# Kernel optimization log

Hardware: AMD Instinct MI355X
Metric: run time of the kernel (lower is better)

Reference implementation:

```python
import jax, jax.numpy as jnp
from jax import lax
import numpy as np

V, E, L, B = 50257, 512, 2048, 8
BASE_RATIO, MIN_RATIO = 0.5, 0.1

def next_power_of_two(x):
    return 1 if x == 0 else 2 ** ((x - 1).bit_length())

def setup_inputs() -> dict:
    key = jax.random.key(0)
    ks = jax.random.split(key, 9)
    s = 0.02
    return {
        "x": jax.random.randint(ks[0], (B, L), 0, V),
        "Wtok": jax.random.normal(ks[1], (V, E), jnp.float32) * s,
        "Wpos": jax.random.normal(ks[2], (L, E), jnp.float32) * s,
        "Wc1": jax.random.normal(ks[3], (3, E, E), jnp.float32) * s,  # WIO layout
        "bc1": jnp.zeros((E,), jnp.float32),
        "Wc2": jax.random.normal(ks[4], (3, E, E), jnp.float32) * s,
        "bc2": jnp.zeros((E,), jnp.float32),
        "Wp": jax.random.normal(ks[5], (E, E), jnp.float32) * (1.0 / np.sqrt(E)),  # torch Linear weight [out,in]
        "bp": jnp.zeros((E,), jnp.float32),
    }

def _conv1d(h, W, b):
    # h: [B, L, E] (NWC), W: [k, in, out] (WIO), SAME padding == torch padding=1 for k=3
    y = lax.conv_general_dilated(h, W, (1,), "SAME", dimension_numbers=("NWC", "WIO", "NWC"))
    return jax.nn.relu(y + b)

def reference(x, Wtok, Wpos, Wc1, bc1, Wc2, bc2, Wp, bp):
    Bsz, Ls = x.shape
    # token + position embedding
    h = Wtok[x] + Wpos[jnp.arange(Ls)][None, :, :]          # [B, L, E]
    h = _conv1d(h, Wc1, bc1)
    h = _conv1d(h, Wc2, bc2)
    # pad to next power of two along sequence
    P = next_power_of_two(Ls)
    if P > Ls:
        h = jnp.pad(h, ((0, 0), (0, P - Ls), (0, 0)))
    x_fft = jnp.fft.fft(h, axis=1)                          # [B, P, E] complex64
    mag = jnp.abs(x_fft)
    thr = 0.1 * mag.max(axis=1, keepdims=True)
    complexity = (mag > thr).astype(jnp.float32).mean(axis=(1, 2))   # [B]
    ratio = jnp.clip(BASE_RATIO * (1.0 - complexity), MIN_RATIO, 1.0)
    N = jnp.clip((ratio * Ls).astype(jnp.int32), 1, Ls)     # [B] kept freq count
    # vectorized equivalent of the per-sample truncation loop:
    # keep first N[i] frequencies (zero the rest), then ifft with n=Ls
    fmask = jnp.arange(Ls)[None, :] < N[:, None]            # [B, L] bool
    x_fft_c = jnp.where(fmask[:, :, None], x_fft[:, :Ls, :], 0.0)
    x_ifft = jnp.fft.ifft(x_fft_c, n=Ls, axis=1).real.astype(h.dtype)  # [B, L, E]
    out = x_ifft @ Wp.T + bp                                # proj
    # recon_target is the exact same computation in the original module
    recon_target = out
    mask_f = fmask.astype(out.dtype)[:, :, None]            # [B, L, 1]
    diff = jnp.abs(out - recon_target) * mask_f
    denom = mask_f.sum() * E
    loss_recon = diff.sum() / jnp.maximum(denom, 1.0)
    return out, loss_recon
```

## Files before the change

kernel.cpp:

```cpp
#include <hip/hip_runtime.h>
#include <hip/hip_bf16.h>
#include <cstddef>

#define BB 8
#define LL 2048
#define EE 512
#define KCONV 1536
#define LPAD 2050

typedef _Float16 h16;
typedef _Float16 h16x2 __attribute__((ext_vector_type(2)));
typedef _Float16 h16x4 __attribute__((ext_vector_type(4)));
typedef _Float16 h16x8 __attribute__((ext_vector_type(8)));
typedef float    f32x4 __attribute__((ext_vector_type(4)));

static const size_t OFF_WT1  = 0;
static const size_t OFF_WT2  = 1572864;
static const size_t OFF_WPB  = 3145728;
static const size_t OFF_CNT2 = 3670016;
static const size_t OFF_H0P  = 4194304;
static const size_t OFF_H1P  = 20987904;
static const size_t OFF_H2T  = 37781504;
static const size_t OFF_XF   = 4194304;
static const size_t OFF_H3E  = 54558720;
static const size_t OFF_H3T  = 20987904;
static const size_t WS_NEED  = 71335936;

__device__ __forceinline__ int padi(int i) { return i + (i >> 5); }
__device__ __forceinline__ int dr5(int n) {
    return ((n & 3) << 8) | (((n >> 2) & 3) << 6) | (((n >> 4) & 3) << 4)
         | (((n >> 6) & 3) << 2) | ((n >> 8) & 3);
}
#define TWOPI_2048 0.0030679616f

__global__ __launch_bounds__(256) void prep_embed_kernel(
    const float* __restrict__ Wc1, const float* __restrict__ Wc2,
    const float* __restrict__ Wp,
    h16* __restrict__ Wt1, h16* __restrict__ Wt2, h16* __restrict__ Wpb,
    const int* __restrict__ x, const float* __restrict__ Wtok,
    const float* __restrict__ Wpos, h16* __restrict__ h0p, h16* __restrict__ h1p)
{
    int blk = blockIdx.x, t = threadIdx.x;
    __shared__ float tl[64][65];
    if (blk < 384) {
        const float* src = (blk < 192) ? Wc1 : Wc2;
        h16* dst = (blk < 192) ? Wt1 : Wt2;
        int tile = blk % 192;
        int o0 = (tile / 24) * 64, r0 = (tile % 24) * 64;
        #pragma unroll
        for (int it = 0; it < 4; ++it) {
            int idx = it * 256 + t;
            int rr = idx >> 4, oo4 = (idx & 15) * 4;
            f32x4 v = *(const f32x4*)(src + (size_t)(r0 + rr) * 512 + o0 + oo4);
            tl[rr][oo4] = v[0]; tl[rr][oo4 + 1] = v[1];
            tl[rr][oo4 + 2] = v[2]; tl[rr][oo4 + 3] = v[3];
        }
        __syncthreads();
        #pragma unroll
        for (int it = 0; it < 4; ++it) {
            int idx = it * 256 + t;
            int oo = idx & 63, rr4 = (idx >> 6) * 4;
            h16x4 v;
            v.x = (h16)tl[rr4][oo]; v.y = (h16)tl[rr4 + 1][oo];
            v.z = (h16)tl[rr4 + 2][oo]; v.w = (h16)tl[rr4 + 3][oo];
            *(h16x4*)(dst + (size_t)(o0 + oo) * 1536 + r0 + rr4) = v;
        }
    } else if (blk < 448) {
        int base = (blk - 384) * 4096;
        #pragma unroll
        for (int i = 0; i < 4; ++i) {
            int idx = base + (i * 256 + t) * 4;
            f32x4 a = *(const f32x4*)(Wp + idx);
            h16x4 v; v.x = (h16)a[0]; v.y = (h16)a[1]; v.z = (h16)a[2]; v.w = (h16)a[3];
            *(h16x4*)(Wpb + idx) = v;
        }
    } else {
        int rowg = (blk - 448) * 4 + (t >> 6);
        int b = rowg / LPAD, r = rowg % LPAD;
        int lane = t & 63;
        size_t o = (size_t)rowg * 512 + lane * 8;
        if (r == 0 || r == LPAD - 1) {
            h16x8 z;
            #pragma unroll
            for (int j = 0; j < 8; ++j) z[j] = (h16)0.f;
            *(h16x8*)(h0p + o) = z;
            *(h16x8*)(h1p + o) = z;
        } else {
            int l = r - 1;
            int tok = x[b * LL + l];
            const f32x4* wt = (const f32x4*)(Wtok + (size_t)tok * 512 + lane * 8);
            const f32x4* wp = (const f32x4*)(Wpos + (size_t)l * 512 + lane * 8);
            f32x4 a0 = wt[0], a1 = wt[1], p0 = wp[0], p1 = wp[1];
            h16x8 v;
            #pragma unroll
            for (int j = 0; j < 4; ++j) v[j] = (h16)(a0[j] + p0[j]);
            #pragma unroll
            for (int j = 0; j < 4; ++j) v[4 + j] = (h16)(a1[j] + p1[j]);
            *(h16x8*)(h0p + o) = v;
        }
    }
}

template<int KTOT, bool RELU, bool TRANSOUT, typename OT>
__global__ __launch_bounds__(512) void gemm3_kernel(
    const h16* __restrict__ A, int a_extra,
    const h16* __restrict__ Bt, const float* __restrict__ bias,
    OT* __restrict__ out, int out_extra, int out_off,
    float* __restrict__ tail)
{
    extern __shared__ __align__(16) h16 lds[];
    const int NKT = KTOT / 64;

    int t = threadIdx.x;
    int w = t >> 6, ln = t & 63;
    int mt = blockIdx.x, nt = blockIdx.y;
    int b = mt >> 3;
    const h16* Ab = A + (size_t)mt * (256 * 512) + (size_t)b * a_extra;
    const h16* Bb = Bt + (size_t)nt * 128 * KTOT;

    int srow = t >> 3;
    int scol = (t & 7) * 8;
    int wr = (w >> 1) * 64, wc = (w & 1) * 64;
    int fr = ln & 15, fg = (ln >> 4) * 8;

    f32x4 acc[4][4];
    #pragma unroll
    for (int m = 0; m < 4; ++m)
        #pragma unroll
        for (int n = 0; n < 4; ++n) acc[m][n] = {0.f, 0.f, 0.f, 0.f};

#define STAGE3(KT, BUF)                                                          \
    {                                                                            \
        int k0_ = (KT) * 64;                                                     \
        h16* sa_ = lds + (BUF) * 16384;                                          \
        h16* sb_ = lds + 49152 + (BUF) * 8192;                                   \
        _Pragma("unroll")                                                        \
        for (int q = 0; q < 4; ++q) {                                            \
            int row_ = q * 64 + srow;                                            \
            int sc_ = scol ^ ((row_ & 7) << 3);                                  \
            __builtin_amdgcn_global_load_lds(                                    \
                (const __attribute__((address_space(1))) unsigned int*)(Ab + (size_t)row_ * 512 + k0_ + sc_), \
                (__attribute__((address_space(3))) unsigned int*)(sa_ + row_ * 64 + scol), \
                16, 0, 0);                                                       \
        }                                                                        \
        _Pragma("unroll")                                                        \
        for (int q = 0; q < 2; ++q) {                                            \
            int row_ = q * 64 + srow;                                            \
            int sc_ = scol ^ ((row_ & 7) << 3);                                  \
            __builtin_amdgcn_global_load_lds(                                    \
                (const __attribute__((address_space(1))) unsigned int*)(Bb + (size_t)row_ * KTOT + k0_ + sc_), \
                (__attribute__((address_space(3))) unsigned int*)(sb_ + row_ * 64 + scol), \
                16, 0, 0);                                                       \
        }                                                                        \
    }

    STAGE3(0, 0);
    STAGE3(1, 1);
    asm volatile("s_waitcnt vmcnt(6)" ::: "memory");
    __builtin_amdgcn_s_barrier();
    __builtin_amdgcn_sched_barrier(0);

    int c = 0;
    for (int kt = 0; kt < NKT; ++kt) {
        int c2 = c + 2; if (c2 >= 3) c2 -= 3;
        if (kt + 2 < NKT) STAGE3(kt + 2, c2);
        const h16* sa = lds + c * 16384;
        const h16* sb = lds + 49152 + c * 8192;
        #pragma unroll
        for (int kk = 0; kk < 64; kk += 32) {
            h16x8 af[4], bf[4];
            #pragma unroll
            for (int m = 0; m < 4; ++m) {
                int arow = wr + m * 16 + fr;
                af[m] = *(const h16x8*)(sa + arow * 64 + ((kk + fg) ^ ((arow & 7) << 3)));
            }
            #pragma unroll
            for (int n = 0; n < 4; ++n) {
                int brow = wc + n * 16 + fr;
                bf[n] = *(const h16x8*)(sb + brow * 64 + ((kk + fg) ^ ((brow & 7) << 3)));
            }
            __builtin_amdgcn_s_setprio(1);
            #pragma unroll
            for (int m = 0; m < 4; ++m)
                #pragma unroll
                for (int n = 0; n < 4; ++n)
                    acc[m][n] = __builtin_amdgcn_mfma_f32_16x16x32_f16(af[m], bf[n], acc[m][n], 0, 0, 0);
            __builtin_amdgcn_s_setprio(0);
        }
        if (kt + 1 < NKT) {
            if (kt + 2 < NKT) { asm volatile("s_waitcnt vmcnt(6)" ::: "memory"); }
            else              { asm volatile("s_waitcnt vmcnt(0)" ::: "memory"); }
            __builtin_amdgcn_s_barrier();
            __builtin_amdgcn_sched_barrier(0);
        }
        c = c + 1; if (c >= 3) c -= 3;
    }
#undef STAGE3

    int fq = (ln >> 4) * 4;
    if constexpr (TRANSOUT) {
        int mtl = (mt & 7) * 256;
        #pragma unroll
        for (int n = 0; n < 4; ++n) {
            int col = nt * 128 + wc + n * 16 + fr;
            float bv = bias[col];
            #pragma unroll
            for (int m = 0; m < 4; ++m) {
                h16x4 hv;
                #pragma unroll
                for (int r = 0; r < 4; ++r) {
                    float xv = acc[m][n][r] + bv;
                    if (RELU) xv = fmaxf(xv, 0.f);
                    hv[r] = (h16)xv;
                }
                int l0a = mtl + wr + m * 16 + fq;
                *(h16x4*)((h16*)out + ((size_t)(b * 512 + col)) * 2048 + l0a) = hv;
            }
        }
    } else {
        #pragma unroll
        for (int n = 0; n < 4; ++n) {
            int col = nt * 128 + wc + n * 16 + fr;
            float bv = bias[col];
            #pragma unroll
            for (int m = 0; m < 4; ++m) {
                #pragma unroll
                for (int r = 0; r < 4; ++r) {
                    int grow = wr + m * 16 + fq + r;
                    float v = acc[m][n][r] + bv;
                    if (RELU) v = fmaxf(v, 0.f);
                    size_t oi = (size_t)(mt * 256 + grow) * 512 + (size_t)b * out_extra + out_off + col;
                    out[oi] = (OT)v;
                }
            }
        }
    }
    if (tail && mt == 0 && nt == 0 && t == 0) tail[0] = 0.f;
}

__global__ __launch_bounds__(256) void fft_fwd_kernel(
    const h16* __restrict__ h2t, h16x2* __restrict__ Xf, int* __restrict__ cnt2)
{
    __shared__ float sre[1056], sim[1056];
    __shared__ float red[4]; __shared__ int redc[4];
    int t = threadIdx.x;
    int b = blockIdx.x >> 9, e = blockIdx.x & 511;
    const h16* src = h2t + ((size_t)b * 512 + e) * 2048;
    #pragma unroll
    for (int j = 0; j < 2; ++j) {
        int n0 = j * 512 + t * 2;
        h16x4 v = *(const h16x4*)(src + n0 * 2);
        int d0 = padi(dr5(n0)), d1 = padi(dr5(n0 + 1));
        sre[d0] = (float)v.x; sim[d0] = (float)v.y;
        sre[d1] = (float)v.z; sim[d1] = (float)v.w;
    }
    __syncthreads();
    #pragma unroll
    for (int s = 0; s < 5; ++s) {
        int L = 1 << (2 * s);
        int K = 512 >> (2 * s);
        int p = t & (L - 1);
        int base = (t >> (2 * s)) * 4 * L + p;
        float th = (float)(p * K) * TWOPI_2048;
        float s1, c1;
        __sincosf(th, &s1, &c1);
        float c2 = 1.f - 2.f * s1 * s1, s2 = 2.f * s1 * c1;
        float c3 = c1 * c2 - s1 * s2,  s3 = s1 * c2 + c1 * s2;
        int i0 = padi(base), i1 = padi(base + L), i2 = padi(base + 2 * L), i3 = padi(base + 3 * L);
        float x0r = sre[i0], x0i = sim[i0];
        float x1r = sre[i1], x1i = sim[i1];
        float x2r = sre[i2], x2i = sim[i2];
        float x3r = sre[i3], x3i = sim[i3];
        float t1r = x1r * c1 + x1i * s1, t1i = x1i * c1 - x1r * s1;
        float t2r = x2r * c2 + x2i * s2, t2i = x2i * c2 - x2r * s2;
        float t3r = x3r * c3 + x3i * s3, t3i = x3i * c3 - x3r * s3;
        float ar = x0r + t2r, ai = x0i + t2i;
        float cr = x0r - t2r, ci = x0i - t2i;
        float br_ = t1r + t3r, bi_ = t1i + t3i;
        float dr_ = t1r - t3r, di_ = t1i - t3i;
        sre[i0] = ar + br_; sim[i0] = ai + bi_;
        sre[i2] = ar - br_; sim[i2] = ai - bi_;
        sre[i1] = cr + di_; sim[i1] = ci - dr_;
        sre[i3] = cr - di_; sim[i3] = ci + dr_;
        __syncthreads();
    }
    size_t xb = ((size_t)b * 512 + e) * 1024;
    float m_a, m_b, m_c, m_d, m_e = 0.f;
    {
        int k = t;
        int km = (1024 - k) & 1023;
        float vkr = sre[padi(k)],  vki = sim[padi(k)];
        float vmr = sre[padi(km)], vmi = sim[padi(km)];
        float p2r = 0.5f * (vkr + vmr), p2i = 0.5f * (vki - vmi);
        float gr  = 0.5f * (vkr - vmr), gi  = 0.5f * (vki + vmi);
        float sn, c;
        __sincosf((float)k * TWOPI_2048, &sn, &c);
        float rr = gr * c + gi * sn, ri = gi * c - gr * sn;
        float x0r = p2r + ri, x0i = p2i - rr;
        float x1r = p2r - ri, x1i = -p2i - rr;
        h16x2 o0; o0.x = (h16)x0r; o0.y = (h16)x0i;
        Xf[xb + k] = o0;
        m_a = x0r * x0r + x0i * x0i;
        m_b = x1r * x1r + x1i * x1i;
        if (k != 0) { h16x2 o1; o1.x = (h16)x1r; o1.y = (h16)x1i; Xf[xb + 1024 - k] = o1; }
    }
    {
        int k = t + 256;
        int km = 1024 - k;
        float vkr = sre[padi(k)],  vki = sim[padi(k)];
        float vmr = sre[padi(km)], vmi = sim[padi(km)];
        float p2r = 0.5f * (vkr + vmr), p2i = 0.5f * (vki - vmi);
        float gr  = 0.5f * (vkr - vmr), gi  = 0.5f * (vki + vmi);
        float sn, c;
        __sincosf((float)k * TWOPI_2048, &sn, &c);
        float rr = gr * c + gi * sn, ri = gi * c - gr * sn;
        float x0r = p2r + ri, x0i = p2i - rr;
        float x1r = p2r - ri, x1i = -p2i - rr;
        h16x2 o0; o0.x = (h16)x0r; o0.y = (h16)x0i;
        Xf[xb + k] = o0;
        h16x2 o1; o1.x = (h16)x1r; o1.y = (h16)x1i;
        Xf[xb + 1024 - k] = o1;
        m_c = x0r * x0r + x0i * x0i;
        m_d = x1r * x1r + x1i * x1i;
    }
    if (t == 0) {
        float vr = sre[padi(512)], vi = sim[padi(512)];
        h16x2 o; o.x = (h16)vr; o.y = (h16)(-vi);
        Xf[xb + 512] = o;
        m_e = vr * vr + vi * vi;
    }
    float lmax = fmaxf(fmaxf(fmaxf(m_a, m_b), fmaxf(m_c, m_d)), m_e);
    #pragma unroll
    for (int off = 32; off; off >>= 1) lmax = fmaxf(lmax, __shfl_xor(lmax, off));
    if ((t & 63) == 0) red[t >> 6] = lmax;
    __syncthreads();
    float thr = 0.01f * fmaxf(fmaxf(red[0], red[1]), fmaxf(red[2], red[3]));
    int wa = (t == 0) ? 1 : 2;
    int c = wa * ((m_a > thr) ? 1 : 0) + wa * ((m_b > thr) ? 1 : 0)
          + 2 * ((m_c > thr) ? 1 : 0) + 2 * ((m_d > thr) ? 1 : 0)
          + 2 * ((m_e > thr) ? 1 : 0);
    #pragma unroll
    for (int off = 32; off; off >>= 1) c += __shfl_xor(c, off);
    if ((t & 63) == 0) redc[t >> 6] = c;
    __syncthreads();
    if (t == 0) cnt2[blockIdx.x] = redc[0] + redc[1] + redc[2] + redc[3];
}

__global__ __launch_bounds__(256) void ifft_kernel(
    const h16x2* __restrict__ Xf, const int* __restrict__ cnt2, h16* __restrict__ h3e)
{
    __shared__ float sre[1056], sim[1056];
    __shared__ int redc[4];
    int t = threadIdx.x;
    int b = blockIdx.x >> 9, e = blockIdx.x & 511;
    int cA = cnt2[b * 512 + t] + cnt2[b * 512 + 256 + t];
    #pragma unroll
    for (int off = 32; off; off >>= 1) cA += __shfl_xor(cA, off);
    if ((t & 63) == 0) redc[t >> 6] = cA;
    __syncthreads();
    int Nb;
    {
        int tot = redc[0] + redc[1] + redc[2] + redc[3];
        float cc = (float)tot * (1.0f / 1048576.0f);
        float ratio = 0.5f * (1.f - cc);
        ratio = fminf(fmaxf(ratio, 0.1f), 1.f);
        int n = (int)(ratio * 2048.f);
        Nb = n < 1 ? 1 : (n > 2048 ? 2048 : n);
    }
    size_t xb = ((size_t)b * 512 + e) * 1024;
    #pragma unroll
    for (int j = 0; j < 2; ++j) {
        int k0 = j * 512 + 2 * t;
        h16x4 v = *(const h16x4*)((const h16*)(Xf + xb + k0));
        bool kp0 = k0 < Nb, kp1 = (k0 + 1) < Nb;
        float sc0 = (k0 == 0) ? (1.0f / 2048.0f) : (1.0f / 4096.0f);
        int p0 = padi(k0), p1 = padi(k0 + 1);
        sre[p0] = kp0 ? (float)v.x * sc0 : 0.f;
        sim[p0] = kp0 ? (float)v.y * sc0 : 0.f;
        sre[p1] = kp1 ? (float)v.z * (1.0f / 4096.0f) : 0.f;
        sim[p1] = kp1 ? (float)v.w * (1.0f / 4096.0f) : 0.f;
    }
    __syncthreads();
    float u0r, u0i, u0pr = 0.f, u0pi = 0.f, u1r, u1i, u1pr, u1pi, u2r = 0.f, u2i = 0.f;
    {
        int k = t;
        if (k == 0) {
            float wr = sre[padi(0)], wi = sim[padi(0)];
            u0r = wr - wi; u0i = wi + wr;
        } else {
            int km = 1024 - k;
            float akr = sre[padi(k)],  aki = sim[padi(k)];
            float bkr = sre[padi(km)], bki = sim[padi(km)];
            float pr = akr + bkr, pi = aki - bki;
            float gr = akr - bkr, gi = aki + bki;
            float sn, c;
            __sincosf((float)k * TWOPI_2048, &sn, &c);
            float qr = gr * c - gi * sn, qi = gi * c + gr * sn;
            u0r = pr - qi; u0i = pi + qr;
            u0pr = pr + qi; u0pi = qr - pi;
        }
    }
    {
        int k = t + 256;
        int km = 1024 - k;
        float akr = sre[padi(k)],  aki = sim[padi(k)];
        float bkr = sre[padi(km)], bki = sim[padi(km)];
        float pr = akr + bkr, pi = aki - bki;
        float gr = akr - bkr, gi = aki + bki;
        float sn, c;
        __sincosf((float)k * TWOPI_2048, &sn, &c);
        float qr = gr * c - gi * sn, qi = gi * c + gr * sn;
        u1r = pr - qi; u1i = pi + qr;
        u1pr = pr + qi; u1pi = qr - pi;
    }
    if (t == 0) {
        float ar = sre[padi(512)], ai = sim[padi(512)];
        u2r = 2.f * ar; u2i = -2.f * ai;
    }
    __syncthreads();
    {
        int d = padi(dr5(t)); sre[d] = u0r; sim[d] = u0i;
        if (t != 0) { int dp = padi(dr5(1024 - t)); sre[dp] = u0pr; sim[dp] = u0pi; }
        int d1 = padi(dr5(t + 256)); sre[d1] = u1r; sim[d1] = u1i;
        int dp1 = padi(dr5(768 - t)); sre[dp1] = u1pr; sim[dp1] = u1pi;
        if (t == 0) { int d2 = padi(dr5(512)); sre[d2] = u2r; sim[d2] = u2i; }
    }
    __syncthreads();
    #pragma unroll
    for (int s = 0; s < 5; ++s) {
        int L = 1 << (2 * s);
        int K = 512 >> (2 * s);
        int p = t & (L - 1);
        int base = (t >> (2 * s)) * 4 * L + p;
        float th = (float)(p * K) * TWOPI_2048;
        float s1, c1;
        __sincosf(th, &s1, &c1);
        float c2 = 1.f - 2.f * s1 * s1, s2 = 2.f * s1 * c1;
        float c3 = c1 * c2 - s1 * s2,  s3 = s1 * c2 + c1 * s2;
        int i0 = padi(base), i1 = padi(base + L), i2 = padi(base + 2 * L), i3 = padi(base + 3 * L);
        float x0r = sre[i0], x0i = sim[i0];
        float x1r = sre[i1], x1i = sim[i1];
        float x2r = sre[i2], x2i = sim[i2];
        float x3r = sre[i3], x3i = sim[i3];
        float t1r = x1r * c1 - x1i * s1, t1i = x1i * c1 + x1r * s1;
        float t2r = x2r * c2 - x2i * s2, t2i = x2i * c2 + x2r * s2;
        float t3r = x3r * c3 - x3i * s3, t3i = x3i * c3 + x3r * s3;
        float ar = x0r + t2r, ai = x0i + t2i;
        float cr = x0r - t2r, ci = x0i - t2i;
        float br_ = t1r + t3r, bi_ = t1i + t3i;
        float dr_ = t1r - t3r, di_ = t1i - t3i;
        sre[i0] = ar + br_; sim[i0] = ai + bi_;
        sre[i2] = ar - br_; sim[i2] = ai - bi_;
        sre[i1] = cr - di_; sim[i1] = ci + dr_;
        sre[i3] = cr + di_; sim[i3] = ci - dr_;
        __syncthreads();
    }
    h16x2* drow = (h16x2*)(h3e + ((size_t)b * 512 + e) * 2048);
    #pragma unroll
    for (int j = 0; j < 4; ++j) {
        int n = j * 256 + t;
        h16x2 o; o.x = (h16)sre[padi(n)]; o.y = (h16)sim[padi(n)];
        drow[n] = o;
    }
}

__global__ __launch_bounds__(256) void trans_kernel(
    const h16* __restrict__ h3e, h16* __restrict__ h3t)
{
    __shared__ h16 tl[64][68];
    int t = threadIdx.x;
    int blk = blockIdx.x;
    int b = blk >> 8, r = blk & 255;
    int e0 = (r >> 5) * 64, l0 = (r & 31) * 64;
    #pragma unroll
    for (int it = 0; it < 4; ++it) {
        int idx = it * 256 + t;
        int er = idx >> 4, lc = (idx & 15) * 4;
        h16x4 v = *(const h16x4*)(h3e + ((size_t)(b * 512 + e0 + er)) * 2048 + l0 + lc);
        tl[er][lc] = v.x; tl[er][lc + 1] = v.y; tl[er][lc + 2] = v.z; tl[er][lc + 3] = v.w;
    }
    __syncthreads();
    #pragma unroll
    for (int it = 0; it < 4; ++it) {
        int idx = it * 256 + t;
        int lr = idx >> 4, ec = (idx & 15) * 4;
        h16x4 v;
        v.x = tl[ec][lr]; v.y = tl[ec + 1][lr]; v.z = tl[ec + 2][lr]; v.w = tl[ec + 3][lr];
        *(h16x4*)(h3t + ((size_t)(b * 2048 + l0 + lr)) * 512 + e0 + ec) = v;
    }
}

extern "C" void kernel_launch(void* const* d_in, const int* in_sizes, int n_in,
                              void* d_out, int out_size, void* d_ws, size_t ws_size,
                              hipStream_t stream)
{
    const int*   x    = (const int*)d_in[0];
    const float* Wtok = (const float*)d_in[1];
    const float* Wpos = (const float*)d_in[2];
    const float* Wc1  = (const float*)d_in[3];
    const float* bc1  = (const float*)d_in[4];
    const float* Wc2  = (const float*)d_in[5];
    const float* bc2  = (const float*)d_in[6];
    const float* Wp   = (const float*)d_in[7];
    const float* bp   = (const float*)d_in[8];
    float* out = (float*)d_out;

    char* ws = (char*)d_ws;
    if (ws_size < WS_NEED) {
        hipMemsetAsync(d_out, 0xFF, 4, stream);
        return;
    }
    h16*   Wt1  = (h16*)(ws + OFF_WT1);
    h16*   Wt2  = (h16*)(ws + OFF_WT2);
    h16*   Wpb  = (h16*)(ws + OFF_WPB);
    int*   cnt2 = (int*)(ws + OFF_CNT2);
    h16*   h0p  = (h16*)(ws + OFF_H0P);
    h16*   h1p  = (h16*)(ws + OFF_H1P);
    h16*   h2t  = (h16*)(ws + OFF_H2T);
    h16x2* Xf   = (h16x2*)(ws + OFF_XF);
    h16*   h3e  = (h16*)(ws + OFF_H3E);
    h16*   h3t  = (h16*)(ws + OFF_H3T);

    const int GEMM_LDS = 3 * (256 * 64 + 128 * 64) * (int)sizeof(h16);

    hipFuncSetAttribute((const void*)&gemm3_kernel<KCONV, true, false, h16>,
                        hipFuncAttributeMaxDynamicSharedMemorySize, GEMM_LDS);
    hipFuncSetAttribute((const void*)&gemm3_kernel<KCONV, true, true, h16>,
                        hipFuncAttributeMaxDynamicSharedMemorySize, GEMM_LDS);
    hipFuncSetAttribute((const void*)&gemm3_kernel<512, false, false, float>,
                        hipFuncAttributeMaxDynamicSharedMemorySize, GEMM_LDS);

    prep_embed_kernel<<<4548, 256, 0, stream>>>(
        Wc1, Wc2, Wp, Wt1, Wt2, Wpb, x, Wtok, Wpos, h0p, h1p);
    gemm3_kernel<KCONV, true, false, h16><<<dim3(64, 4), 512, GEMM_LDS, stream>>>(
        h0p, 1024, Wt1, bc1, h1p, 1024, 512, nullptr);
    gemm3_kernel<KCONV, true, true, h16><<<dim3(64, 4), 512, GEMM_LDS, stream>>>(
        h1p, 1024, Wt2, bc2, h2t, 0, 0, nullptr);
    fft_fwd_kernel<<<4096, 256, 0, stream>>>(h2t, Xf, cnt2);
    ifft_kernel<<<4096, 256, 0, stream>>>(Xf, cnt2, h3e);
    trans_kernel<<<2048, 256, 0, stream>>>(h3e, h3t);
    gemm3_kernel<512, false, false, float><<<dim3(64, 4), 512, GEMM_LDS, stream>>>(
        h3t, 0, Wpb, bp, out, 0, 0, out + (size_t)BB * LL * EE);
}
```

Measured before the change: 131.3 us.

## Software-pipeline LDS fragment reads across K-tiles with a 2x unrolled loop

Unrolls the GEMM K loop by two and splits each 64-wide K tile into two 32-wide halves with separate fragment registers. The first-half fragments of the next tile are read from LDS before the barrier, so those reads overlap the wait rather than following it. The cost is higher register pressure. There is also a hazard: the next buffer is read after only a per-thread vmcnt wait and before the workgroup barrier, so data loaded by other waves may not be visible yet. The loop also assumes an even tile count.

```diff
diff --git a/kernel.cpp b/kernel.cpp
--- a/kernel.cpp
+++ b/kernel.cpp
@@ -154,48 +154,70 @@
         }                                                                        \
     }
 
+#define RDFRAG_H(BUF, H, AF, BF)                                                 \
+    {                                                                            \
+        const h16* sa_ = lds + (BUF) * 16384;                                    \
+        const h16* sb_ = lds + 49152 + (BUF) * 8192;                             \
+        _Pragma("unroll")                                                        \
+        for (int m = 0; m < 4; ++m) {                                            \
+            int arow = wr + m * 16 + fr;                                         \
+            AF[m] = *(const h16x8*)(sa_ + arow * 64 + (((H) * 32 + fg) ^ ((arow & 7) << 3))); \
+        }                                                                        \
+        _Pragma("unroll")                                                        \
+        for (int n = 0; n < 4; ++n) {                                            \
+            int brow = wc + n * 16 + fr;                                         \
+            BF[n] = *(const h16x8*)(sb_ + brow * 64 + (((H) * 32 + fg) ^ ((brow & 7) << 3))); \
+        }                                                                        \
+    }
+
+#define MFMA_H(AF, BF)                                                           \
+    {                                                                            \
+        __builtin_amdgcn_s_setprio(1);                                           \
+        _Pragma("unroll")                                                        \
+        for (int m = 0; m < 4; ++m)                                              \
+            _Pragma("unroll")                                                    \
+            for (int n = 0; n < 4; ++n)                                          \
+                acc[m][n] = __builtin_amdgcn_mfma_f32_16x16x32_f16(AF[m], BF[n], acc[m][n], 0, 0, 0); \
+        __builtin_amdgcn_s_setprio(0);                                           \
+    }
+
+    h16x8 afX[4], bfX[4], afY[4], bfY[4], af1[4], bf1[4];
+
     STAGE3(0, 0);
     STAGE3(1, 1);
     asm volatile("s_waitcnt vmcnt(6)" ::: "memory");
     __builtin_amdgcn_s_barrier();
     __builtin_amdgcn_sched_barrier(0);
-
-    int c = 0;
-    for (int kt = 0; kt < NKT; ++kt) {
-        int c2 = c + 2; if (c2 >= 3) c2 -= 3;
-        if (kt + 2 < NKT) STAGE3(kt + 2, c2);
-        const h16* sa = lds + c * 16384;
-        const h16* sb = lds + 49152 + c * 8192;
-        #pragma unroll
-        for (int kk = 0; kk < 64; kk += 32) {
-            h16x8 af[4], bf[4];
-            #pragma unroll
-            for (int m = 0; m < 4; ++m) {
-                int arow = wr + m * 16 + fr;
-                af[m] = *(const h16x8*)(sa + arow * 64 + ((kk + fg) ^ ((arow & 7) << 3)));
-            }
-            #pragma unroll
-            for (int n = 0; n < 4; ++n) {
-                int brow = wc + n * 16 + fr;
-                bf[n] = *(const h16x8*)(sb + brow * 64 + ((kk + fg) ^ ((brow & 7) << 3)));
-            }
-            __builtin_amdgcn_s_setprio(1);
-            #pragma unroll
-            for (int m = 0; m < 4; ++m)
-                #pragma unroll
-                for (int n = 0; n < 4; ++n)
-                    acc[m][n] = __builtin_amdgcn_mfma_f32_16x16x32_f16(af[m], bf[n], acc[m][n], 0, 0, 0);
-            __builtin_amdgcn_s_setprio(0);
-        }
-        if (kt + 1 < NKT) {
-            if (kt + 2 < NKT) { asm volatile("s_waitcnt vmcnt(6)" ::: "memory"); }
+    RDFRAG_H(0, 0, afX, bfX);
+
+    for (int kt = 0; kt < NKT; kt += 2) {
+        int c0 = kt % 3, c1 = (kt + 1) % 3, cs2 = (kt + 2) % 3, cs3 = (kt + 3) % 3;
+        if (kt + 2 < NKT) STAGE3(kt + 2, cs2);
+        RDFRAG_H(c0, 1, af1, bf1);
+        MFMA_H(afX, bfX);
+        MFMA_H(af1, bf1);
+        if (kt + 2 < NKT) { asm volatile("s_waitcnt vmcnt(6)" ::: "memory"); }
+        else              { asm volatile("s_waitcnt vmcnt(0)" ::: "memory"); }
+        RDFRAG_H(c1, 0, afY, bfY);
+        __builtin_amdgcn_sched_barrier(0);
+        __builtin_amdgcn_s_barrier();
+        __builtin_amdgcn_sched_barrier(0);
+        if (kt + 3 < NKT) STAGE3(kt + 3, cs3);
+        RDFRAG_H(c1, 1, af1, bf1);
+        MFMA_H(afY, bfY);
+        MFMA_H(af1, bf1);
+        if (kt + 2 < NKT) {
+            if (kt + 3 < NKT) { asm volatile("s_waitcnt vmcnt(6)" ::: "memory"); }
             else              { asm volatile("s_waitcnt vmcnt(0)" ::: "memory"); }
+            RDFRAG_H(cs2, 0, afX, bfX);
+            __builtin_amdgcn_sched_barrier(0);
             __builtin_amdgcn_s_barrier();
             __builtin_amdgcn_sched_barrier(0);
         }
-        c = c + 1; if (c >= 3) c -= 3;
     }
 #undef STAGE3
+#undef RDFRAG_H
+#undef MFMA_H
 
     int fq = (ln >> 4) * 4;
     if constexpr (TRANSOUT) {
```

Result: no change. 131.0 us (-0.2%).
